# Kernel tuning notes

Hardware: AMD Instinct MI355X
Metric: run time of the kernel (lower is better)

The kernel has to match this reference:

```python
import jax, jax.numpy as jnp
import numpy as np

B = 2          # batch
L = 2048       # seq len
D_MODEL = 1024
D_INNER = 2 * D_MODEL   # expand = 2
D_STATE = 16
D_CONV = 4
DT_RANK = D_MODEL // 16  # 64


def setup_inputs() -> dict:
    key = jax.random.key(0)
    kx, kf, kb = jax.random.split(key, 3)
    d = {"x": jax.random.normal(kx, (B, L, D_MODEL), jnp.float32)}
    for pre, k in (("f_", kf), ("b_", kb)):
        kk = jax.random.split(k, 6)
        d[pre + "in_proj_w"] = jax.random.normal(kk[0], (2 * D_INNER, D_MODEL), jnp.float32) * 0.02
        d[pre + "conv_w"] = jax.random.normal(kk[1], (D_INNER, 1, D_CONV), jnp.float32) * 0.2
        d[pre + "conv_b"] = jnp.zeros((D_INNER,), jnp.float32)
        d[pre + "x_proj_w"] = jax.random.normal(kk[2], (DT_RANK + 2 * D_STATE, D_INNER), jnp.float32) * 0.02
        d[pre + "dt_proj_w"] = jax.random.normal(kk[3], (D_INNER, DT_RANK), jnp.float32) * 0.02
        # dt bias init so softplus(bias) ~ dt in [exp(-4), exp(-2)] range (mamba-style)
        d[pre + "dt_proj_b"] = jax.random.uniform(kk[4], (D_INNER,), jnp.float32, minval=-4.0, maxval=-2.0)
        # S4D-real init: A = -[1..d_state]
        d[pre + "A_log"] = jnp.log(jnp.broadcast_to(jnp.arange(1, D_STATE + 1, dtype=jnp.float32), (D_INNER, D_STATE)))
        d[pre + "D"] = jnp.ones((D_INNER,), jnp.float32)
        d[pre + "out_proj_w"] = jax.random.normal(kk[5], (D_MODEL, D_INNER), jnp.float32) * 0.02
    return d


def _silu(x):
    return x * jax.nn.sigmoid(x)


def _selective_scan(u, dt, A, Bm, Cm, Dp):
    # u, dt: [B, L, d_inner]; Bm, Cm: [B, L, d_state]; A: [d_inner, d_state]; Dp: [d_inner]
    def step(h, inp):
        u_t, dt_t, B_t, C_t = inp                       # [B,d], [B,d], [B,n], [B,n]
        dA = jnp.exp(dt_t[..., None] * A)               # [B, d, n]  (ZOH discretization)
        dBu = dt_t[..., None] * B_t[:, None, :] * u_t[..., None]
        h = dA * h + dBu                                # [B, d, n]
        y = jnp.einsum('bdn,bn->bd', h, C_t)            # [B, d]
        return h, y

    h0 = jnp.zeros((u.shape[0], A.shape[0], A.shape[1]), u.dtype)
    xs = (jnp.swapaxes(u, 0, 1), jnp.swapaxes(dt, 0, 1),
          jnp.swapaxes(Bm, 0, 1), jnp.swapaxes(Cm, 0, 1))
    _, ys = jax.lax.scan(step, h0, xs)                  # ys: [L, B, d_inner]
    return jnp.swapaxes(ys, 0, 1) + u * Dp              # skip connection D*u


def _mamba(x, in_proj_w, conv_w, conv_b, x_proj_w, dt_proj_w, dt_proj_b, A_log, Dp, out_proj_w):
    # x: [B, L, d_model]
    xz = x @ in_proj_w.T                                # [B, L, 2*d_inner]
    xi, z = jnp.split(xz, 2, axis=-1)
    # depthwise causal conv1d, kernel D_CONV, output truncated to L (left pad)
    xc = jax.lax.conv_general_dilated(
        jnp.swapaxes(xi, 1, 2), conv_w, (1,), [(D_CONV - 1, 0)],
        dimension_numbers=('NCH', 'OIH', 'NCH'), feature_group_count=D_INNER)
    xi = _silu(jnp.swapaxes(xc, 1, 2) + conv_b)         # [B, L, d_inner]
    x_dbl = xi @ x_proj_w.T                             # [B, L, dt_rank + 2*d_state]
    dt, Bm, Cm = jnp.split(x_dbl, [DT_RANK, DT_RANK + D_STATE], axis=-1)
    dt = jax.nn.softplus(dt @ dt_proj_w.T + dt_proj_b)  # [B, L, d_inner]
    A = -jnp.exp(A_log)                                 # [d_inner, d_state]
    y = _selective_scan(xi, dt, A, Bm, Cm, Dp)
    y = y * _silu(z)                                    # gated
    return y @ out_proj_w.T                             # [B, L, d_model]


def reference(x,
              f_in_proj_w, f_conv_w, f_conv_b, f_x_proj_w, f_dt_proj_w, f_dt_proj_b, f_A_log, f_D, f_out_proj_w,
              b_in_proj_w, b_conv_w, b_conv_b, b_x_proj_w, b_dt_proj_w, b_dt_proj_b, b_A_log, b_D, b_out_proj_w):
    h_fwd = _mamba(x, f_in_proj_w, f_conv_w, f_conv_b, f_x_proj_w,
                   f_dt_proj_w, f_dt_proj_b, f_A_log, f_D, f_out_proj_w)
    h_bwd = _mamba(jnp.flip(x, axis=1), b_in_proj_w, b_conv_w, b_conv_b, b_x_proj_w,
                   b_dt_proj_w, b_dt_proj_b, b_A_log, b_D, b_out_proj_w)
    h_bwd = jnp.flip(h_bwd, axis=1)
    return jnp.concatenate([h_fwd, h_bwd], axis=-1)     # [B, L, 2*d_model]
```

## Files before the change

kernel.cpp:

```cpp
#include <hip/hip_runtime.h>

#define BB 2
#define LL 2048
#define DM 1024
#define DI 2048
#define NTOK (BB*LL)
#define NC 32
#define CL (LL/NC)
#define NCH (BB*DI)

typedef __bf16 bf16x8 __attribute__((ext_vector_type(8)));
typedef float f32x4 __attribute__((ext_vector_type(4)));
typedef int i32x4 __attribute__((ext_vector_type(4)));

#define LOG2E 1.44269504088896340736f

__device__ __forceinline__ float siluf(float x){ return x / (1.f + __expf(-x)); }
__device__ __forceinline__ float softplusf(float x){
  if (x > 20.f) return x;
  return log1pf(__expf(x));
}
__device__ __forceinline__ unsigned short f2bf(float f){
  unsigned int u = __builtin_bit_cast(unsigned int, f);
  u += 0x7fffu + ((u >> 16) & 1u);
  return (unsigned short)(u >> 16);
}
__device__ __forceinline__ float bf2f(unsigned short u){
  return __builtin_bit_cast(float, (unsigned int)u << 16);
}
template<typename CT>
__device__ __forceinline__ void st_ct(CT* p, float v){
  if constexpr (sizeof(CT)==2) *p = (CT)f2bf(v); else *p = (CT)v;
}

__device__ __forceinline__ void gl_lds16(const unsigned short* g, unsigned short* l){
  __builtin_amdgcn_global_load_lds(
      (const __attribute__((address_space(1))) void*)g,
      (__attribute__((address_space(3))) void*)l, 16, 0, 0);
}

#define SEG0 4096
#define SEG1 8192
#define SEG2 512
#define SEG3 256
#define SEG4 4096
#define CAST_BLOCKS (SEG0+SEG1+SEG2+SEG3+SEG4)

__device__ __forceinline__ void cast4(const float* src, unsigned short* dst){
  float4 v = *reinterpret_cast<const float4*>(src);
  ushort4 o; o.x=f2bf(v.x); o.y=f2bf(v.y); o.z=f2bf(v.z); o.w=f2bf(v.w);
  *reinterpret_cast<ushort4*>(dst) = o;
}

__global__ __launch_bounds__(256) void k_cast_all(
    const float* __restrict__ x,
    const float* __restrict__ ipw0, const float* __restrict__ ipw1,
    const float* __restrict__ xpw0, const float* __restrict__ xpw1,
    const float* __restrict__ dtw0, const float* __restrict__ dtw1,
    const float* __restrict__ opw0, const float* __restrict__ opw1,
    unsigned short* __restrict__ x_bf, unsigned short* __restrict__ w_bf,
    unsigned short* __restrict__ wpad, unsigned short* __restrict__ dtw_bf,
    unsigned short* __restrict__ outw){
  int bid = blockIdx.x;
  int ti = threadIdx.x*4;
  if (bid < SEG0){
    int i = bid*1024 + ti;
    cast4(x + i, x_bf + i);
  } else if (bid < SEG0+SEG1){
    int i = (bid-SEG0)*1024 + ti;
    const int n = (2*DI)*DM;
    const float* src = (i < n) ? ipw0 : ipw1;
    int off = (i < n) ? i : i - n;
    cast4(src + off, w_bf + i);
  } else if (bid < SEG0+SEG1+SEG2){
    int i = (bid-SEG0-SEG1)*1024 + ti;
    const int ntotal = 128*DI, nreal = 96*DI;
    int dir = i / ntotal;
    int r = i - dir*ntotal;
    if (r < nreal){
      cast4((dir ? xpw1 : xpw0) + r, wpad + i);
    } else {
      ushort4 z{0,0,0,0};
      *reinterpret_cast<ushort4*>(wpad + i) = z;
    }
  } else if (bid < SEG0+SEG1+SEG2+SEG3){
    int i = (bid-SEG0-SEG1-SEG2)*1024 + ti;
    const int n = DI*64;
    const float* src = (i < n) ? dtw0 : dtw1;
    int off = (i < n) ? i : i - n;
    cast4(src + off, dtw_bf + i);
  } else {
    int i = (bid-SEG0-SEG1-SEG2-SEG3)*1024 + ti;
    const int n = DM*DI;
    const float* src = (i < n) ? opw0 : opw1;
    int off = (i < n) ? i : i - n;
    cast4(src + off, outw + i);
  }
}

template<int NT>
__global__ __launch_bounds__(512) void k_gemm256(
    const unsigned short* __restrict__ A, int lda,
    const unsigned short* __restrict__ Bw, int ldb, long long bz,
    unsigned short* __restrict__ C, unsigned short* __restrict__ C2, int nsplit,
    int ldc, long long cz){
  __shared__ unsigned short L[2*32768];
  const int dir = blockIdx.z;
  Bw += (size_t)dir*bz;
  const int m0 = blockIdx.y*256;
  const int bn0 = blockIdx.x*256;
  unsigned short* Cout; int n0;
  if (bn0 < nsplit){ Cout = C; n0 = bn0; } else { Cout = C2; n0 = bn0 - nsplit; }
  Cout += (size_t)dir*cz;

  const int tid = threadIdx.x;
  const int w = tid >> 6, lane = tid & 63;
  const int rT = tid >> 3;
  const int sG = (tid & 7) ^ (rT & 7);
  const unsigned short* srcA = A  + (size_t)(m0  + rT)*lda + sG*8;
  const unsigned short* srcB = Bw + (size_t)(bn0 + rT)*ldb + sG*8;
  unsigned short* const lw = &L[w*512];
  const int wmb = (w>>2)*128, wnb = (w&3)*64;
  const int fr = lane & 15;
  const int sK0 = ((lane>>4) ^ (lane&7))*8;

  f32x4 acc[8][4] = {};

  auto STAGE = [&](int kt, int c){
    const unsigned short* a_ = srcA + kt*64;
    const unsigned short* b_ = srcB + kt*64;
    unsigned short* l_ = lw + c*32768;
    gl_lds16(a_,                   l_);
    gl_lds16(a_ + (size_t)64*lda,  l_ + 4096);
    gl_lds16(a_ + (size_t)128*lda, l_ + 8192);
    gl_lds16(a_ + (size_t)192*lda, l_ + 12288);
    gl_lds16(b_,                   l_ + 16384);
    gl_lds16(b_ + (size_t)64*ldb,  l_ + 20480);
    gl_lds16(b_ + (size_t)128*ldb, l_ + 24576);
    gl_lds16(b_ + (size_t)192*ldb, l_ + 28672);
  };
  auto COMPUTE = [&](int c){
    const unsigned short* base = &L[c*32768];
#pragma unroll
    for (int kk=0; kk<2; kk++){
      const int sk = sK0 ^ (kk<<5);
      bf16x8 a[8], b[4];
#pragma unroll
      for (int i=0;i<8;i++)
        a[i] = *reinterpret_cast<const bf16x8*>(&base[(wmb + i*16 + fr)*64 + sk]);
#pragma unroll
      for (int j=0;j<4;j++)
        b[j] = *reinterpret_cast<const bf16x8*>(&base[16384 + (wnb + j*16 + fr)*64 + sk]);
#pragma unroll
      for (int i=0;i<8;i++)
#pragma unroll
        for (int j=0;j<4;j++)
          acc[i][j] = __builtin_amdgcn_mfma_f32_16x16x32_bf16(a[i], b[j], acc[i][j], 0,0,0);
    }
  };

  STAGE(0, 0);
  STAGE(1, 1);
#pragma unroll 2
  for (int t = 0; t < NT-2; ++t){
    asm volatile("s_waitcnt vmcnt(8)" ::: "memory");
    asm volatile("s_barrier" ::: "memory");
    COMPUTE(t & 1);
    asm volatile("s_waitcnt lgkmcnt(0)" ::: "memory");
    asm volatile("s_barrier" ::: "memory");
    STAGE(t+2, t & 1);
  }
  asm volatile("s_waitcnt vmcnt(8)" ::: "memory");
  asm volatile("s_barrier" ::: "memory");
  COMPUTE(NT & 1);
  asm volatile("s_waitcnt vmcnt(0)" ::: "memory");
  asm volatile("s_barrier" ::: "memory");
  COMPUTE((NT-1) & 1);

  const int er = (lane>>4)*4;
#pragma unroll
  for (int i=0;i<8;i++)
#pragma unroll
    for (int j=0;j<4;j++){
      int row = m0 + wmb + i*16 + er;
      int col = n0 + wnb + j*16 + fr;
      unsigned short* cp = Cout + (size_t)row*ldc + col;
#pragma unroll
      for (int r=0;r<4;r++) cp[(size_t)r*ldc] = f2bf(acc[i][j][r]);
    }
}

template<int EPI, int KSPLIT, typename CT>
__global__ __launch_bounds__(256) void k_gemm_bt(
    const unsigned short* __restrict__ A, int lda, long long az,
    const unsigned short* __restrict__ Bw, int ldb, long long bz,
    CT* __restrict__ C, CT* __restrict__ C2, int nsplit,
    int ldc, long long cz, int coffz,
    int K, int coff,
    const float* __restrict__ bias0, const float* __restrict__ bias1){
  __shared__ unsigned short As[128*32];
  __shared__ unsigned short Bs[128*32];
  const int z = blockIdx.z;
  const int dirz = z / KSPLIT, kc = z - dirz*KSPLIT;
  A  += (size_t)dirz*az + (size_t)kc*K;
  Bw += (size_t)dirz*bz + (size_t)kc*K;
  const int bn0 = blockIdx.x*128;
  int n0 = bn0;
  if (bn0 >= nsplit){ C = C2; n0 = bn0 - nsplit; }
  C  += (size_t)z*cz;
  const int co = coff + dirz*coffz;
  const float* bias = dirz ? bias1 : bias0;

  const int t = threadIdx.x;
  const int m0 = blockIdx.y*128;
  const int lane = t & 63, w = t >> 6;
  const int wm = (w>>1)*64, wn = (w&1)*64;

  const int gr = lane >> 2;
  const int gslot = (lane & 3) ^ ((lane >> 3) & 3);
  const unsigned short* gA = A  + (size_t)(m0  + 32*w + gr)*lda + gslot*8;
  const unsigned short* gB = Bw + (size_t)(bn0 + 32*w + gr)*ldb + gslot*8;
  unsigned short* lA = &As[(32*w)*32];
  unsigned short* lB = &Bs[(32*w)*32];

  f32x4 acc[4][4] = {};
  const int fr = lane & 15;
  const int rslot = ((lane>>4) ^ ((lane>>1)&3))*8;

  for (int k0=0; k0<K; k0+=32){
    __syncthreads();
    gl_lds16(gA + k0, lA);
    gl_lds16(gA + (size_t)16*lda + k0, lA + 16*32);
    gl_lds16(gB + k0, lB);
    gl_lds16(gB + (size_t)16*ldb + k0, lB + 16*32);
    __syncthreads();
    bf16x8 af[4], bfr[4];
#pragma unroll
    for (int i=0;i<4;i++){
      af[i]  = *reinterpret_cast<const bf16x8*>(&As[(wm + i*16 + fr)*32 + rslot]);
      bfr[i] = *reinterpret_cast<const bf16x8*>(&Bs[(wn + i*16 + fr)*32 + rslot]);
    }
#pragma unroll
    for (int i=0;i<4;i++)
#pragma unroll
      for (int j=0;j<4;j++)
        acc[i][j] = __builtin_amdgcn_mfma_f32_16x16x32_bf16(af[i], bfr[j], acc[i][j], 0,0,0);
  }
  const int er = (lane>>4)*4;
#pragma unroll
  for (int i=0;i<4;i++)
#pragma unroll
    for (int j=0;j<4;j++){
      int row = m0 + wm + i*16 + er;
      int bcol = n0 + wn + j*16 + fr;
      CT* cp = C + (size_t)row*ldc + co + bcol;
      if (EPI == 1){
        float bv = bias[bcol];
#pragma unroll
        for (int r=0;r<4;r++) st_ct(&cp[(size_t)r*ldc], softplusf(acc[i][j][r] + bv));
      } else {
#pragma unroll
        for (int r=0;r<4;r++) st_ct(&cp[(size_t)r*ldc], acc[i][j][r]);
      }
    }
}

__global__ __launch_bounds__(256) void k_conv_silu(const unsigned short* __restrict__ xpre,
    const float* __restrict__ cw0, const float* __restrict__ cw1,
    const float* __restrict__ cb0, const float* __restrict__ cb1,
    unsigned short* __restrict__ xi_bf){
  const int dir = blockIdx.z;
  const int d0 = threadIdx.x*8;
  const int tok0 = blockIdx.x*4;
  const int b = tok0 >> 11;
  const int t0 = tok0 & (LL-1);
  const float* cw = dir ? cw1 : cw0;
  const float* cb = dir ? cb1 : cb0;
  const unsigned short* xpd = xpre + (size_t)dir*NTOK*DI;
  unsigned short* outp = xi_bf + (size_t)dir*NTOK*DI;

  float wv[4][8];
#pragma unroll
  for (int c=0;c<8;c++){
    float4 w = *reinterpret_cast<const float4*>(cw + (size_t)(d0+c)*4);
    wv[0][c]=w.x; wv[1][c]=w.y; wv[2][c]=w.z; wv[3][c]=w.w;
  }
  float bv[8];
  {
    float4 b0 = *reinterpret_cast<const float4*>(cb + d0);
    float4 b1 = *reinterpret_cast<const float4*>(cb + d0 + 4);
    bv[0]=b0.x; bv[1]=b0.y; bv[2]=b0.z; bv[3]=b0.w;
    bv[4]=b1.x; bv[5]=b1.y; bv[6]=b1.z; bv[7]=b1.w;
  }
  const int rbase = t0 + (dir ? 0 : -3);
  float rows[7][8];
#pragma unroll
  for (int i=0;i<7;i++){
    int r = rbase + i;
    if (r >= 0 && r < LL){
      union { i32x4 v; unsigned short u[8]; } x;
      x.v = *reinterpret_cast<const i32x4*>(xpd + ((size_t)b*LL + r)*DI + d0);
#pragma unroll
      for (int c=0;c<8;c++) rows[i][c] = bf2f(x.u[c]);
    } else {
#pragma unroll
      for (int c=0;c<8;c++) rows[i][c] = 0.f;
    }
  }
#pragma unroll
  for (int j=0;j<4;j++){
    union { i32x4 v; unsigned short u[8]; } o;
#pragma unroll
    for (int c=0;c<8;c++){
      float acc = bv[c];
#pragma unroll
      for (int m=0;m<4;m++){
        float w = dir ? wv[3-m][c] : wv[m][c];
        acc += w * rows[j+m][c];
      }
      o.u[c] = f2bf(siluf(acc));
    }
    *reinterpret_cast<i32x4*>(outp + ((size_t)(tok0+j))*DI + d0) = o.v;
  }
}

__global__ __launch_bounds__(256) void k_xred(const float* __restrict__ part,
    float* __restrict__ xdbl, unsigned short* __restrict__ xdbl_bf){
  int idx = blockIdx.x*256 + threadIdx.x;
  if (idx >= 2*NTOK*96) return;
  int dir = idx / (NTOK*96);
  int rem = idx - dir*(NTOK*96);
  int tok = rem / 96, j = rem - tok*96;
  const float* pd = part + (size_t)dir*4*NTOK*128;
  const size_t czs = (size_t)NTOK*128;
  size_t o = (size_t)tok*128 + j;
  float v = pd[o] + pd[czs + o] + pd[2*czs + o] + pd[3*czs + o];
  xdbl[(size_t)dir*NTOK*96 + (size_t)tok*96 + j] = v;
  if (j < 64) xdbl_bf[(size_t)dir*NTOK*64 + (size_t)tok*64 + j] = f2bf(v);
}

__global__ __launch_bounds__(256) void k_scan_p1(const unsigned short* __restrict__ u,
    const unsigned short* __restrict__ dt, const float* __restrict__ xdbl,
    const float* __restrict__ A_log0, const float* __restrict__ A_log1,
    float* __restrict__ prodA, float* __restrict__ hloc){
  __shared__ float Bs[CL*16];
  const int dir = blockIdx.z;
  u    += (size_t)dir*NTOK*DI;
  dt   += (size_t)dir*NTOK*DI;
  xdbl += (size_t)dir*NTOK*96;
  prodA += (size_t)dir*NC*NCH*16;
  hloc  += (size_t)dir*NC*NCH*16;
  const float* A_log = dir ? A_log1 : A_log0;
  const int tid = threadIdx.x;
  const int ch = blockIdx.x*256 + tid;
  const int c = blockIdx.y;
  const int b = (blockIdx.x*256) >> 11;
  const int d = ch & (DI-1);
  for (int i = tid; i < CL*16; i += 256){
    int s = i >> 4, j = i & 15;
    int sg = c*CL + s;
    int tt = dir ? (LL-1-sg) : sg;
    Bs[i] = xdbl[((size_t)b*LL + tt)*96 + 64 + j];
  }
  float Alog2[16];
  {
    const float4* ap = reinterpret_cast<const float4*>(A_log + (size_t)d*16);
#pragma unroll
    for (int q=0;q<4;q++){
      float4 v = ap[q];
      Alog2[q*4+0] = -__expf(v.x)*LOG2E;
      Alog2[q*4+1] = -__expf(v.y)*LOG2E;
      Alog2[q*4+2] = -__expf(v.z)*LOG2E;
      Alog2[q*4+3] = -__expf(v.w)*LOG2E;
    }
  }
  __syncthreads();
  float h[16], pa[16];
#pragma unroll
  for (int n=0;n<16;n++){ h[n]=0.f; pa[n]=1.f; }
  int tok0 = b*LL + (dir ? (LL-1-c*CL) : c*CL);
  const unsigned short* up = u + (size_t)tok0*DI + d;
  const unsigned short* dtp = dt + (size_t)tok0*DI + d;
  const ptrdiff_t stp = dir ? -(ptrdiff_t)DI : (ptrdiff_t)DI;
#pragma unroll 2
  for (int s=0; s<CL; s++){
    float uv  = bf2f(*up); up += stp;
    float dtv = bf2f(*dtp); dtp += stp;
    float dtu = dtv*uv;
    const f32x4* br = reinterpret_cast<const f32x4*>(&Bs[s*16]);
    f32x4 B0=br[0], B1=br[1], B2=br[2], B3=br[3];
#pragma unroll
    for (int n=0;n<16;n++){
      float dA = __builtin_amdgcn_exp2f(dtv*Alog2[n]);
      float Bv = (n<4)?B0[n&3] : (n<8)?B1[n&3] : (n<12)?B2[n&3] : B3[n&3];
      h[n] = dA*h[n] + dtu*Bv;
      pa[n] *= dA;
    }
  }
  float* pp = prodA + ((size_t)c*NCH + ch)*16;
  float* hp = hloc  + ((size_t)c*NCH + ch)*16;
#pragma unroll
  for (int q=0;q<4;q++){
    *reinterpret_cast<f32x4*>(pp + q*4) = f32x4{pa[q*4],pa[q*4+1],pa[q*4+2],pa[q*4+3]};
    *reinterpret_cast<f32x4*>(hp + q*4) = f32x4{h[q*4],h[q*4+1],h[q*4+2],h[q*4+3]};
  }
}

__global__ __launch_bounds__(256) void k_scan_comb(float* __restrict__ prodA,
    const float* __restrict__ hloc){
  int i = blockIdx.x*256 + threadIdx.x;
  int dir = i / (NCH*16);
  int j = i - dir*(NCH*16);
  float* pa = prodA + (size_t)dir*NC*NCH*16;
  const float* hl = hloc + (size_t)dir*NC*NCH*16;
  float hs = 0.f;
#pragma unroll
  for (int c=0; c<NC; c++){
    size_t idx = (size_t)c*NCH*16 + j;
    float p = pa[idx], h = hl[idx];
    pa[idx] = hs;
    hs = p*hs + h;
  }
}

__global__ __launch_bounds__(256) void k_scan_p2(unsigned short* __restrict__ uy,
    const unsigned short* __restrict__ dt, const float* __restrict__ xdbl,
    const unsigned short* __restrict__ zbuf,
    const float* __restrict__ A_log0, const float* __restrict__ A_log1,
    const float* __restrict__ Dp0, const float* __restrict__ Dp1,
    const float* __restrict__ hstart){
  __shared__ float BCs[CL*32];
  const int dir = blockIdx.z;
  uy   += (size_t)dir*NTOK*DI;
  dt   += (size_t)dir*NTOK*DI;
  zbuf += (size_t)dir*NTOK*DI;
  xdbl += (size_t)dir*NTOK*96;
  hstart += (size_t)dir*NC*NCH*16;
  const float* A_log = dir ? A_log1 : A_log0;
  const float* Dp = dir ? Dp1 : Dp0;
  const int tid = threadIdx.x;
  const int ch = blockIdx.x*256 + tid;
  const int c = blockIdx.y;
  const int b = (blockIdx.x*256) >> 11;
  const int d = ch & (DI-1);
  for (int i = tid; i < CL*32; i += 256){
    int s = i >> 5, j = i & 31;
    int sg = c*CL + s;
    int tt = dir ? (LL-1-sg) : sg;
    BCs[i] = xdbl[((size_t)b*LL + tt)*96 + 64 + j];
  }
  float Alog2[16];
  {
    const float4* ap = reinterpret_cast<const float4*>(A_log + (size_t)d*16);
#pragma unroll
    for (int q=0;q<4;q++){
      float4 v = ap[q];
      Alog2[q*4+0] = -__expf(v.x)*LOG2E;
      Alog2[q*4+1] = -__expf(v.y)*LOG2E;
      Alog2[q*4+2] = -__expf(v.z)*LOG2E;
      Alog2[q*4+3] = -__expf(v.w)*LOG2E;
    }
  }
  float h[16];
  {
    const float* hp = hstart + ((size_t)c*NCH + ch)*16;
#pragma unroll
    for (int q=0;q<4;q++){
      f32x4 v = *reinterpret_cast<const f32x4*>(hp + q*4);
      h[q*4]=v[0]; h[q*4+1]=v[1]; h[q*4+2]=v[2]; h[q*4+3]=v[3];
    }
  }
  const float Dval = Dp[d];
  __syncthreads();
  int tok0 = b*LL + (dir ? (LL-1-c*CL) : c*CL);
  unsigned short* up = uy + (size_t)tok0*DI + d;
  const unsigned short* zp = zbuf + (size_t)tok0*DI + d;
  const unsigned short* dtp = dt + (size_t)tok0*DI + d;
  const ptrdiff_t stp = dir ? -(ptrdiff_t)DI : (ptrdiff_t)DI;
#pragma unroll 2
  for (int s=0; s<CL; s++){
    float uv  = bf2f(*up);
    float zv  = bf2f(*zp); zp += stp;
    float dtv = bf2f(*dtp); dtp += stp;
    float dtu = dtv*uv;
    float y = Dval*uv;
    const f32x4* br = reinterpret_cast<const f32x4*>(&BCs[s*32]);
    f32x4 B0=br[0], B1=br[1], B2=br[2], B3=br[3];
    f32x4 C0=br[4], C1=br[5], C2=br[6], C3=br[7];
#pragma unroll
    for (int n=0;n<16;n++){
      float dA = __builtin_amdgcn_exp2f(dtv*Alog2[n]);
      float Bv = (n<4)?B0[n&3] : (n<8)?B1[n&3] : (n<12)?B2[n&3] : B3[n&3];
      float Cv = (n<4)?C0[n&3] : (n<8)?C1[n&3] : (n<12)?C2[n&3] : C3[n&3];
      h[n] = dA*h[n] + dtu*Bv;
      y += h[n]*Cv;
    }
    *up = f2bf(y * siluf(zv)); up += stp;
  }
}

extern "C" void kernel_launch(void* const* d_in, const int* in_sizes, int n_in,
                              void* d_out, int out_size, void* d_ws, size_t ws_size,
                              hipStream_t stream){
  (void)in_sizes; (void)n_in; (void)out_size; (void)ws_size;
  const float* x = (const float*)d_in[0];
  const float* ipw[2], *cw[2], *cb[2], *xpw[2], *dtw_[2], *dtb[2], *Alog[2], *Dp[2], *opw[2];
  for (int dir=0; dir<2; dir++){
    ipw[dir]  = (const float*)d_in[1 + dir*9 + 0];
    cw[dir]   = (const float*)d_in[1 + dir*9 + 1];
    cb[dir]   = (const float*)d_in[1 + dir*9 + 2];
    xpw[dir]  = (const float*)d_in[1 + dir*9 + 3];
    dtw_[dir] = (const float*)d_in[1 + dir*9 + 4];
    dtb[dir]  = (const float*)d_in[1 + dir*9 + 5];
    Alog[dir] = (const float*)d_in[1 + dir*9 + 6];
    Dp[dir]   = (const float*)d_in[1 + dir*9 + 7];
    opw[dir]  = (const float*)d_in[1 + dir*9 + 8];
  }
  char* p = (char*)d_ws;
  auto alloc = [&](size_t bytes)->void*{ void* r=(void*)p; p += (bytes+255)&~(size_t)255; return r; };
  unsigned short* x_bf   = (unsigned short*)alloc((size_t)NTOK*DM*2);
  unsigned short* w_bf   = (unsigned short*)alloc((size_t)2*(2*DI)*DM*2);
  float* part            = (float*)w_bf;
  unsigned short* xpre   = (unsigned short*)alloc((size_t)2*NTOK*DI*2);
  float* prodA           = (float*)xpre;
  float* hloc            = (float*)(xpre + (size_t)NTOK*DI);
  unsigned short* zbuf   = (unsigned short*)alloc((size_t)2*NTOK*DI*2);
  unsigned short* xi_bf  = (unsigned short*)alloc((size_t)2*NTOK*DI*2);
  float* xdbl            = (float*)alloc((size_t)2*NTOK*96*4);
  unsigned short* xdbl_bf= (unsigned short*)alloc((size_t)2*NTOK*64*2);
  unsigned short* dt_bf  = (unsigned short*)alloc((size_t)2*NTOK*DI*2);
  unsigned short* wpad   = (unsigned short*)alloc((size_t)2*128*DI*2);
  unsigned short* dtw_bf = (unsigned short*)alloc((size_t)2*DI*64*2);
  unsigned short* outw   = (unsigned short*)alloc((size_t)2*DM*DI*2);

  k_cast_all<<<CAST_BLOCKS, 256, 0, stream>>>(
      x, ipw[0], ipw[1], xpw[0], xpw[1], dtw_[0], dtw_[1], opw[0], opw[1],
      x_bf, w_bf, wpad, dtw_bf, outw);

  k_gemm256<16><<<dim3(16,16,2), 512, 0, stream>>>(
      x_bf, DM, w_bf, DM, (long long)(2*DI)*DM,
      xpre, zbuf, DI, DI, (long long)NTOK*DI);
  k_conv_silu<<<dim3(NTOK/4,1,2), 256, 0, stream>>>(xpre, cw[0], cw[1], cb[0], cb[1], xi_bf);
  k_gemm_bt<0,4,float><<<dim3(1,32,8), 256, 0, stream>>>(
      xi_bf, DI, (long long)NTOK*DI, wpad, DI, (long long)128*DI,
      part, part, 1<<30, 128, (long long)NTOK*128, 0, 512, 0, nullptr, nullptr);
  k_xred<<<(2*NTOK*96+255)/256, 256, 0, stream>>>(part, xdbl, xdbl_bf);
  k_gemm_bt<1,1,unsigned short><<<dim3(16,32,2), 256, 0, stream>>>(
      xdbl_bf, 64, (long long)NTOK*64, dtw_bf, 64, (long long)DI*64,
      dt_bf, dt_bf, 1<<30, DI, (long long)NTOK*DI, 0, 64, 0, dtb[0], dtb[1]);
  k_scan_p1<<<dim3(NCH/256, NC, 2), 256, 0, stream>>>(xi_bf, dt_bf, xdbl, Alog[0], Alog[1], prodA, hloc);
  k_scan_comb<<<2*NCH*16/256, 256, 0, stream>>>(prodA, hloc);
  k_scan_p2<<<dim3(NCH/256, NC, 2), 256, 0, stream>>>(xi_bf, dt_bf, xdbl, zbuf,
      Alog[0], Alog[1], Dp[0], Dp[1], prodA);
  k_gemm_bt<0,1,float><<<dim3(8,32,2), 256, 0, stream>>>(
      xi_bf, DI, (long long)NTOK*DI, outw, DI, (long long)DM*DI,
      (float*)d_out, (float*)d_out, 1<<30, 2*DM, 0, DM, DI, 0, nullptr, nullptr);
}
```

Before: 384.6 us.

## Replace stored chunk decay products with dt sums and double scan chunk count

The chunked selective scan no longer accumulates and stores 16 per-state decay products per channel and chunk. Pass 1 now stores only the per-chunk sum of dt, and the combine kernel rebuilds each product as exp2(sum_dt * A). This works because the product of exp(dt*A) over a chunk equals exp(A * sum dt), so it cuts multiplies in pass 1 and memory traffic through the combine. The chunk count also goes from 32 to 64, doubling the blocks available in both scan passes but making the serial combine loop longer. Both buffers now sit at fixed offsets at the start of the workspace, reusing regions that are dead by that point in the pipeline.

```diff
diff --git a/kernel.cpp b/kernel.cpp
--- a/kernel.cpp
+++ b/kernel.cpp
@@ -5,7 +5,7 @@
 #define DM 1024
 #define DI 2048
 #define NTOK (BB*LL)
-#define NC 32
+#define NC 64
 #define CL (LL/NC)
 #define NCH (BB*DI)
 
@@ -342,14 +342,12 @@
 __global__ __launch_bounds__(256) void k_scan_p1(const unsigned short* __restrict__ u,
     const unsigned short* __restrict__ dt, const float* __restrict__ xdbl,
     const float* __restrict__ A_log0, const float* __restrict__ A_log1,
-    float* __restrict__ prodA, float* __restrict__ hloc){
+    float* __restrict__ hloc, float* __restrict__ dtsum){
   __shared__ float Bs[CL*16];
   const int dir = blockIdx.z;
   u    += (size_t)dir*NTOK*DI;
   dt   += (size_t)dir*NTOK*DI;
   xdbl += (size_t)dir*NTOK*96;
-  prodA += (size_t)dir*NC*NCH*16;
-  hloc  += (size_t)dir*NC*NCH*16;
   const float* A_log = dir ? A_log1 : A_log0;
   const int tid = threadIdx.x;
   const int ch = blockIdx.x*256 + tid;
@@ -375,9 +373,10 @@
     }
   }
   __syncthreads();
-  float h[16], pa[16];
-#pragma unroll
-  for (int n=0;n<16;n++){ h[n]=0.f; pa[n]=1.f; }
+  float h[16];
+#pragma unroll
+  for (int n=0;n<16;n++) h[n]=0.f;
+  float dts = 0.f;
   int tok0 = b*LL + (dir ? (LL-1-c*CL) : c*CL);
   const unsigned short* up = u + (size_t)tok0*DI + d;
   const unsigned short* dtp = dt + (size_t)tok0*DI + d;
@@ -387,6 +386,7 @@
     float uv  = bf2f(*up); up += stp;
     float dtv = bf2f(*dtp); dtp += stp;
     float dtu = dtv*uv;
+    dts += dtv;
     const f32x4* br = reinterpret_cast<const f32x4*>(&Bs[s*16]);
     f32x4 B0=br[0], B1=br[1], B2=br[2], B3=br[3];
 #pragma unroll
@@ -394,32 +394,34 @@
       float dA = __builtin_amdgcn_exp2f(dtv*Alog2[n]);
       float Bv = (n<4)?B0[n&3] : (n<8)?B1[n&3] : (n<12)?B2[n&3] : B3[n&3];
       h[n] = dA*h[n] + dtu*Bv;
-      pa[n] *= dA;
-    }
-  }
-  float* pp = prodA + ((size_t)c*NCH + ch)*16;
-  float* hp = hloc  + ((size_t)c*NCH + ch)*16;
-#pragma unroll
-  for (int q=0;q<4;q++){
-    *reinterpret_cast<f32x4*>(pp + q*4) = f32x4{pa[q*4],pa[q*4+1],pa[q*4+2],pa[q*4+3]};
+    }
+  }
+  float* hp = hloc + (((size_t)(dir*NC + c)*NCH + ch))*16;
+#pragma unroll
+  for (int q=0;q<4;q++)
     *reinterpret_cast<f32x4*>(hp + q*4) = f32x4{h[q*4],h[q*4+1],h[q*4+2],h[q*4+3]};
-  }
-}
-
-__global__ __launch_bounds__(256) void k_scan_comb(float* __restrict__ prodA,
-    const float* __restrict__ hloc){
+  dtsum[(size_t)(dir*NC + c)*NCH + ch] = dts;
+}
+
+__global__ __launch_bounds__(256) void k_scan_comb(float* __restrict__ hloc,
+    const float* __restrict__ dtsum,
+    const float* __restrict__ A_log0, const float* __restrict__ A_log1){
   int i = blockIdx.x*256 + threadIdx.x;
   int dir = i / (NCH*16);
   int j = i - dir*(NCH*16);
-  float* pa = prodA + (size_t)dir*NC*NCH*16;
-  const float* hl = hloc + (size_t)dir*NC*NCH*16;
+  int ch = j >> 4, n = j & 15;
+  int d = ch & (DI-1);
+  const float* A_log = dir ? A_log1 : A_log0;
+  float Alog2 = -__expf(A_log[(size_t)d*16 + n])*LOG2E;
   float hs = 0.f;
-#pragma unroll
+#pragma unroll 4
   for (int c=0; c<NC; c++){
-    size_t idx = (size_t)c*NCH*16 + j;
-    float p = pa[idx], h = hl[idx];
-    pa[idx] = hs;
-    hs = p*hs + h;
+    size_t base = (size_t)(dir*NC + c)*NCH + ch;
+    float pa = __builtin_amdgcn_exp2f(dtsum[base]*Alog2);
+    size_t idx = base*16 + n;
+    float h = hloc[idx];
+    hloc[idx] = hs;
+    hs = pa*hs + h;
   }
 }
 
@@ -435,7 +437,6 @@
   dt   += (size_t)dir*NTOK*DI;
   zbuf += (size_t)dir*NTOK*DI;
   xdbl += (size_t)dir*NTOK*96;
-  hstart += (size_t)dir*NC*NCH*16;
   const float* A_log = dir ? A_log1 : A_log0;
   const float* Dp = dir ? Dp1 : Dp0;
   const int tid = threadIdx.x;
@@ -463,7 +464,7 @@
   }
   float h[16];
   {
-    const float* hp = hstart + ((size_t)c*NCH + ch)*16;
+    const float* hp = hstart + (((size_t)(dir*NC + c)*NCH + ch))*16;
 #pragma unroll
     for (int q=0;q<4;q++){
       f32x4 v = *reinterpret_cast<const f32x4*>(hp + q*4);
@@ -522,8 +523,6 @@
   unsigned short* w_bf   = (unsigned short*)alloc((size_t)2*(2*DI)*DM*2);
   float* part            = (float*)w_bf;
   unsigned short* xpre   = (unsigned short*)alloc((size_t)2*NTOK*DI*2);
-  float* prodA           = (float*)xpre;
-  float* hloc            = (float*)(xpre + (size_t)NTOK*DI);
   unsigned short* zbuf   = (unsigned short*)alloc((size_t)2*NTOK*DI*2);
   unsigned short* xi_bf  = (unsigned short*)alloc((size_t)2*NTOK*DI*2);
   float* xdbl            = (float*)alloc((size_t)2*NTOK*96*4);
@@ -532,6 +531,8 @@
   unsigned short* wpad   = (unsigned short*)alloc((size_t)2*128*DI*2);
   unsigned short* dtw_bf = (unsigned short*)alloc((size_t)2*DI*64*2);
   unsigned short* outw   = (unsigned short*)alloc((size_t)2*DM*DI*2);
+  float* hloc  = (float*)d_ws;
+  float* dtsum = (float*)((char*)d_ws + (size_t)32*1024*1024);
 
   k_cast_all<<<CAST_BLOCKS, 256, 0, stream>>>(
       x, ipw[0], ipw[1], xpw[0], xpw[1], dtw_[0], dtw_[1], opw[0], opw[1],
@@ -548,10 +549,11 @@
   k_gemm_bt<1,1,unsigned short><<<dim3(16,32,2), 256, 0, stream>>>(
       xdbl_bf, 64, (long long)NTOK*64, dtw_bf, 64, (long long)DI*64,
       dt_bf, dt_bf, 1<<30, DI, (long long)NTOK*DI, 0, 64, 0, dtb[0], dtb[1]);
-  k_scan_p1<<<dim3(NCH/256, NC, 2), 256, 0, stream>>>(xi_bf, dt_bf, xdbl, Alog[0], Alog[1], prodA, hloc);
-  k_scan_comb<<<2*NCH*16/256, 256, 0, stream>>>(prodA, hloc);
+  k_scan_p1<<<dim3(NCH/256, NC, 2), 256, 0, stream>>>(xi_bf, dt_bf, xdbl,
+      Alog[0], Alog[1], hloc, dtsum);
+  k_scan_comb<<<2*NCH*16/256, 256, 0, stream>>>(hloc, dtsum, Alog[0], Alog[1]);
   k_scan_p2<<<dim3(NCH/256, NC, 2), 256, 0, stream>>>(xi_bf, dt_bf, xdbl, zbuf,
-      Alog[0], Alog[1], Dp[0], Dp[1], prodA);
+      Alog[0], Alog[1], Dp[0], Dp[1], hloc);
   k_gemm_bt<0,1,float><<<dim3(8,32,2), 256, 0, stream>>>(
       xi_bf, DI, (long long)NTOK*DI, outw, DI, (long long)DM*DI,
       (float*)d_out, (float*)d_out, 1<<30, 2*DM, 0, DM, DI, 0, nullptr, nullptr);
```

Measured after the change: 374.3 us. 1.03x faster.
